# Performance work log

Hardware: AMD Instinct MI355X
Metric: run time of the kernel (lower is better)

## Reference

```python
import jax, jax.numpy as jnp
import numpy as np

WEIGHTS = {'seg': 1.0, 'grid': 0.5, 'baseline': 0.8, 'theta': 0.3, 'signal': 2.0}
IGNORE = 255


def _bce(p, t):
    # torch BCELoss: clamps log terms at -100
    lp = jnp.maximum(jnp.log(jnp.clip(p, 1e-12, 1.0)), -100.0)
    l1p = jnp.maximum(jnp.log(jnp.clip(1.0 - p, 1e-12, 1.0)), -100.0)
    return -(t * lp + (1.0 - t) * l1p).mean()


def _ce_ignore(logits, target):
    # logits (B,C,H,W), target (B,H,W) int; mean over target != 255
    logp = jax.nn.log_softmax(logits, axis=1)
    valid = target != IGNORE
    t_safe = jnp.where(valid, target, 0)
    nll = -jnp.take_along_axis(logp, t_safe[:, None].astype(jnp.int32), axis=1)[:, 0]
    return (nll * valid).sum() / jnp.maximum(valid.sum(), 1)


def _dice(logits, target, num_classes):
    p = jax.nn.softmax(logits, axis=1)                      # (B,C,H,W)
    oh = jax.nn.one_hot(target, num_classes, dtype=p.dtype) # (B,H,W,C)
    oh = jnp.transpose(oh, (0, 3, 1, 2))
    inter = (p * oh).sum(axis=(2, 3))
    union = p.sum(axis=(2, 3)) + oh.sum(axis=(2, 3))
    dice = (2.0 * inter + 1e-07) / (union + 1e-07)
    return 1.0 - dice.mean()


def _resize_bilinear_ac(x, out_h, out_w):
    # align_corners=True bilinear, x: (B,C,H,W)
    B, C, H, Wd = x.shape
    ys = jnp.linspace(0.0, H - 1.0, out_h)
    xs = jnp.linspace(0.0, Wd - 1.0, out_w)
    y0 = jnp.floor(ys).astype(jnp.int32); y1 = jnp.minimum(y0 + 1, H - 1); wy = (ys - y0).astype(x.dtype)
    x0 = jnp.floor(xs).astype(jnp.int32); x1 = jnp.minimum(x0 + 1, Wd - 1); wx = (xs - x0).astype(x.dtype)
    rows = x[:, :, y0, :] * (1 - wy)[None, None, :, None] + x[:, :, y1, :] * wy[None, None, :, None]
    out = rows[:, :, :, x0] * (1 - wx) + rows[:, :, :, x1] * wx
    return out


def _normalize_signal_masked(sig, mask):
    # sig, mask: (B,12,T); per-lead min/max normalize on valid region
    mf = mask.astype(sig.dtype)
    cnt = mf.sum(-1, keepdims=True)
    mn = jnp.min(jnp.where(mask, sig, jnp.inf), -1, keepdims=True)
    mx = jnp.max(jnp.where(mask, sig, -jnp.inf), -1, keepdims=True)
    rng = mx - mn
    ok = (cnt >= 2) & (rng >= 1e-06)
    mn_s = jnp.where(ok, mn, 0.0)
    rng_s = jnp.where(ok, rng, 1.0)
    norm = (2.0 * (sig - mn_s) / (rng_s + 1e-08) - 1.0) * mf
    return jnp.where(ok, norm, 0.0)


def _masked_mae(pred, target, mask):
    mf = mask.astype(pred.dtype)
    return (jnp.abs(pred - target) * mf).sum() / (mf.sum() + 1e-07)


def _masked_pearson(pred, target, mask):
    mf = mask.astype(pred.dtype)
    cnt = mf.sum(-1)                                   # (B,12)
    cs = jnp.maximum(cnt, 1.0)
    pm = (pred * mf).sum(-1) / cs
    tm = (target * mf).sum(-1) / cs
    pc = (pred - pm[..., None]) * mf
    tc = (target - tm[..., None]) * mf
    num = (pc * tc).sum(-1)
    ps = jnp.sqrt((pc ** 2).sum(-1) + 1e-06)
    ts = jnp.sqrt((tc ** 2).sum(-1) + 1e-06)
    corr = jnp.clip(num / (ps * ts + 1e-06), -1.0, 1.0)
    valid = (cnt >= 10).astype(pred.dtype)
    n_valid = valid.sum()
    avg = (corr * valid).sum() / jnp.maximum(n_valid, 1.0)
    return jnp.where(n_valid > 0, 1.0 - avg, 1.0)


def setup_inputs() -> dict:
    key = jax.random.key(0)
    ks = jax.random.split(key, 11)
    B, H, Wd, T = 8, 512, 512, 5000
    return {
        'wave_seg_pred': jax.random.normal(ks[0], (B, 13, H, Wd), jnp.float32),
        'wave_seg_target': jax.random.randint(ks[1], (B, H, Wd), 0, 13, jnp.int32),
        'grid_pred': jax.random.uniform(ks[2], (B, 1, H, Wd), jnp.float32),
        'grid_target': jax.random.uniform(ks[3], (B, 1, H, Wd), jnp.float32),
        'baseline_pred': jax.random.uniform(ks[4], (B, 12, H // 16, Wd // 16), jnp.float32),
        'baseline_target': jax.random.uniform(ks[5], (B, 12, H, Wd), jnp.float32),
        'theta_pred': jax.random.normal(ks[6], (B, 2, 3), jnp.float32),
        'theta_gt': jax.random.normal(ks[7], (B, 2, 3), jnp.float32),
        'signal_pred': jax.random.normal(ks[8], (B, 12, T), jnp.float32),
        'gt_signal': jax.random.normal(ks[9], (B, T, 12), jnp.float32),
        'signal_mask': jax.random.randint(ks[10], (B, T, 12), 0, 2, jnp.int32).astype(bool),
    }


def reference(wave_seg_pred, wave_seg_target, grid_pred, grid_target,
              baseline_pred, baseline_target, theta_pred, theta_gt,
              signal_pred, gt_signal, signal_mask):
    # seg
    seg = (_ce_ignore(wave_seg_pred, wave_seg_target)
           + _dice(wave_seg_pred, wave_seg_target, 13)) * WEIGHTS['seg']
    # grid
    inter = (grid_pred * grid_target).sum()
    union = grid_pred.sum() + grid_target.sum()
    grid = (_bce(grid_pred, grid_target)
            + (1.0 - (2.0 * inter + 1e-07) / (union + 1e-07))) * WEIGHTS['grid']
    # baseline
    Hp, Wp = baseline_pred.shape[2], baseline_pred.shape[3]
    bt = _resize_bilinear_ac(baseline_target, Hp, Wp)
    baseline = _bce(baseline_pred, bt) * WEIGHTS['baseline']
    # theta
    theta = jnp.abs(theta_pred - theta_gt).mean() * WEIGHTS['theta']
    # signal
    sig_t = jnp.swapaxes(gt_signal, 1, 2)     # (B,12,T)
    m = jnp.swapaxes(signal_mask, 1, 2)       # (B,12,T)
    pn = _normalize_signal_masked(signal_pred, m)
    tn = _normalize_signal_masked(sig_t, m)
    signal = (_masked_mae(pn, tn, m) + _masked_pearson(pn, tn, m)) * WEIGHTS['signal']
    total = seg + grid + baseline + theta + signal
    return jnp.stack([seg, grid, baseline, theta, signal, total])
```

## Files before the change

### kernel.cpp

```cpp
#include <hip/hip_runtime.h>
#include <math.h>

#define WS_SEG_NLL    0
#define WS_SEG_VALID  8
#define WS_INTER      16
#define WS_PSUM       120
#define WS_OHCNT      224
#define WS_GRID_BCE   328
#define WS_GRID_INTER 329
#define WS_GRID_PSUM  330
#define WS_GRID_TSUM  331
#define WS_BASE_BCE   332
#define WS_SIG_ABS    333
#define WS_SIG_CNT    334
#define WS_SIG_CORR   335
#define WS_SIG_NV     336
#define WS_MASK_FLAG  337
#define WS_DONE       338
#define WS_SIGSTATS   340
#define WS_FLOATS     820

#define SEG_NB   512
#define GRID_NB  256
#define BASE_NB  384
#define SIGA_NB  96
#define TOTAL_NB (SEG_NB + GRID_NB + BASE_NB + SIGA_NB)

#define AS_GLOBAL const __attribute__((address_space(1))) void*
#define AS_LDS    __attribute__((address_space(3))) void*

__device__ inline float wave_sum(float v) {
    #pragma unroll
    for (int o = 32; o > 0; o >>= 1) v += __shfl_down(v, o, 64);
    return v;
}

template <int OP>
__device__ inline float blk_red(float v, float* sb) {
    #pragma unroll
    for (int o = 32; o > 0; o >>= 1) {
        float u = __shfl_down(v, o, 64);
        v = (OP == 0) ? (v + u) : ((OP == 1) ? fminf(v, u) : fmaxf(v, u));
    }
    __syncthreads();
    if ((threadIdx.x & 63) == 0) sb[threadIdx.x >> 6] = v;
    __syncthreads();
    const int nw = blockDim.x >> 6;
    float r = sb[0];
    for (int w = 1; w < nw; w++) {
        float u = sb[w];
        r = (OP == 0) ? (r + u) : ((OP == 1) ? fminf(r, u) : fmaxf(r, u));
    }
    return r;
}

__device__ void seg_part(int sb_idx, const float* __restrict__ pred,
                         const int* __restrict__ tgt, float* __restrict__ ws) {
    const int b   = sb_idx >> 6;
    const int c64 = sb_idx & 63;
    const int HW  = 262144;
    const float* predf = pred + (size_t)b * 13 * HW;
    const int*   tgtb  = tgt + (size_t)b * HW;

    __shared__ alignas(16) float s_tile[28 * 256];
    int* s_tgt_i = (int*)&s_tile[26 * 256];
    __shared__ float s_inter[13];
    __shared__ float s_psum[13];
    __shared__ int   s_cnt[13];
    __shared__ float s_nll;
    __shared__ float s_nval;
    if (threadIdx.x < 13) { s_inter[threadIdx.x] = 0.f; s_psum[threadIdx.x] = 0.f; s_cnt[threadIdx.x] = 0; }
    if (threadIdx.x == 13) s_nll = 0.f;
    if (threadIdx.x == 14) s_nval = 0.f;

    const int lane = threadIdx.x & 63;
    const int wv   = threadIdx.x >> 6;

    float psum[13];
    #pragma unroll
    for (int c = 0; c < 13; c++) psum[c] = 0.f;
    float nll = 0.f, nval = 0.f;

    #pragma unroll 1
    for (int tile = 0; tile < 8; tile++) {
        const int px0 = c64 * 4096 + tile * 512;
        #pragma unroll
        for (int i = 0; i < 7; i++) {
            const int k = wv * 7 + i;
            const float* g;
            if (k < 26) g = predf + (size_t)(k >> 1) * HW + px0 + (k & 1) * 256;
            else        g = (const float*)(tgtb + px0 + (k - 26) * 256);
            g += lane * 4;
            __builtin_amdgcn_global_load_lds((AS_GLOBAL)g,
                                             (AS_LDS)&s_tile[k * 256], 16, 0, 0);
        }
        __syncthreads();

        #pragma unroll
        for (int kp = 0; kp < 2; kp++) {
            const int p = threadIdx.x + kp * 256;
            const int t = s_tgt_i[p];
            float x[13];
            #pragma unroll
            for (int c = 0; c < 13; c++) x[c] = s_tile[c * 512 + p];
            float m = x[0];
            #pragma unroll
            for (int c = 1; c < 13; c++) m = fmaxf(m, x[c]);
            float xt = x[0];
            #pragma unroll
            for (int c = 1; c < 13; c++) xt = (c == t) ? x[c] : xt;
            float se = 0.f;
            #pragma unroll
            for (int c = 0; c < 13; c++) { x[c] = __expf(x[c] - m); se += x[c]; }
            const float inv = __builtin_amdgcn_rcpf(se);
            #pragma unroll
            for (int c = 0; c < 13; c++) psum[c] += x[c] * inv;
            if ((unsigned)t < 13u) {
                atomicAdd(&s_inter[t], __expf(xt - m) * inv);
                atomicAdd(&s_cnt[t], 1);
                nll  += m + __logf(se) - xt;
                nval += 1.f;
            }
        }
        if (tile < 7) __syncthreads();
    }

    const bool lane0 = (lane == 0);
    #pragma unroll
    for (int c = 0; c < 13; c++) {
        float a = wave_sum(psum[c]);
        if (lane0) atomicAdd(&s_psum[c], a);
    }
    { float a = wave_sum(nll);  if (lane0) atomicAdd(&s_nll, a); }
    { float a = wave_sum(nval); if (lane0) atomicAdd(&s_nval, a); }
    __syncthreads();
    if (threadIdx.x < 13) {
        atomicAdd(&ws[WS_PSUM  + b * 13 + threadIdx.x], s_psum[threadIdx.x]);
        atomicAdd(&ws[WS_INTER + b * 13 + threadIdx.x], s_inter[threadIdx.x]);
        atomicAdd(&ws[WS_OHCNT + b * 13 + threadIdx.x], (float)s_cnt[threadIdx.x]);
    }
    if (threadIdx.x == 64) atomicAdd(&ws[WS_SEG_NLL + b],   s_nll);
    if (threadIdx.x == 65) atomicAdd(&ws[WS_SEG_VALID + b], s_nval);
}

__device__ void grid_part(int gb, const float4* __restrict__ gp,
                          const float4* __restrict__ gt, float* __restrict__ ws) {
    const int N4 = 2097152 / 4;
    float bce = 0.f, inter = 0.f, ps = 0.f, ts = 0.f;
    const int stride = GRID_NB * 256;
    for (int i = gb * 256 + threadIdx.x; i < N4; i += stride) {
        const float4 p4 = gp[i];
        const float4 t4 = gt[i];
        const float pa[4] = {p4.x, p4.y, p4.z, p4.w};
        const float ta[4] = {t4.x, t4.y, t4.z, t4.w};
        #pragma unroll
        for (int k = 0; k < 4; k++) {
            const float p = pa[k], t = ta[k];
            const float pc  = fminf(fmaxf(p, 1e-12f), 1.0f);
            const float qc  = fminf(fmaxf(1.f - p, 1e-12f), 1.0f);
            const float lp  = fmaxf(__logf(pc), -100.f);
            const float l1p = fmaxf(__logf(qc), -100.f);
            bce  -= t * lp + (1.f - t) * l1p;
            inter += p * t;
            ps += p;
            ts += t;
        }
    }
    __shared__ float s4[4];
    if (threadIdx.x < 4) s4[threadIdx.x] = 0.f;
    __syncthreads();
    const bool lane0 = (threadIdx.x & 63) == 0;
    { float a = wave_sum(bce);   if (lane0) atomicAdd(&s4[0], a); }
    { float a = wave_sum(inter); if (lane0) atomicAdd(&s4[1], a); }
    { float a = wave_sum(ps);    if (lane0) atomicAdd(&s4[2], a); }
    { float a = wave_sum(ts);    if (lane0) atomicAdd(&s4[3], a); }
    __syncthreads();
    if (threadIdx.x == 0) {
        atomicAdd(&ws[WS_GRID_BCE],   s4[0]);
        atomicAdd(&ws[WS_GRID_INTER], s4[1]);
        atomicAdd(&ws[WS_GRID_PSUM],  s4[2]);
        atomicAdd(&ws[WS_GRID_TSUM],  s4[3]);
    }
}

__device__ void base_part(int bb, const float* __restrict__ bp,
                          const float* __restrict__ bt, float* __restrict__ ws) {
    const int idx = bb * 256 + threadIdx.x;
    const int w  = idx & 31;
    const int h  = (idx >> 5) & 31;
    const int bc = idx >> 10;
    const float* img = bt + (size_t)bc * 262144;
    const float step = 511.0f / 31.0f;
    const float yy = h * step, xx = w * step;
    int y0 = (int)floorf(yy); int y1 = min(y0 + 1, 511); const float wy = yy - y0;
    int x0 = (int)floorf(xx); int x1 = min(x0 + 1, 511); const float wx = xx - x0;
    const float v00 = img[y0 * 512 + x0], v01 = img[y0 * 512 + x1];
    const float v10 = img[y1 * 512 + x0], v11 = img[y1 * 512 + x1];
    const float r0 = v00 * (1.f - wy) + v10 * wy;
    const float r1 = v01 * (1.f - wy) + v11 * wy;
    const float t  = r0 * (1.f - wx) + r1 * wx;
    const float p  = bp[idx];
    const float pc  = fminf(fmaxf(p, 1e-12f), 1.0f);
    const float qc  = fminf(fmaxf(1.f - p, 1e-12f), 1.0f);
    const float lp  = fmaxf(__logf(pc), -100.f);
    const float l1p = fmaxf(__logf(qc), -100.f);
    const float bce = -(t * lp + (1.f - t) * l1p);

    __shared__ float sb[4];
    const float s = blk_red<0>(bce, sb);
    if (threadIdx.x == 0) atomicAdd(&ws[WS_BASE_BCE], s);
}

__device__ void sigA_part(int sl, const float* __restrict__ sp,
                          const float* __restrict__ st, const void* __restrict__ mp,
                          float* __restrict__ ws) {
    const int T = 5000;
    const int b = sl / 12, l = sl % 12;
    const float* ps = sp + (size_t)(b * 12 + l) * T;
    const float* ts_base = st + (size_t)b * T * 12 + l;
    const int* mi = (const int*)mp;
    const unsigned char* mb = (const unsigned char*)mp;
    const size_t mbase = (size_t)b * T * 12 + l;

    __shared__ float sb[4];
    __shared__ int s_flag;
    if (threadIdx.x == 0) s_flag = 0;
    __syncthreads();
    int f = 0;
    for (int i = threadIdx.x; i < 3072; i += blockDim.x)
        if ((i & 3) && mb[i]) f = 1;
    if (__any(f) && (threadIdx.x & 63) == 0) atomicOr(&s_flag, 1);
    __syncthreads();
    const bool m32 = (s_flag == 0);

    float cnt = 0.f;
    float mnp = __builtin_inff(), mxp = -__builtin_inff();
    float mnt = __builtin_inff(), mxt = -__builtin_inff();
    for (int t = threadIdx.x; t < T; t += blockDim.x) {
        const bool m = m32 ? (mi[mbase + (size_t)t * 12] != 0)
                           : (mb[mbase + (size_t)t * 12] != 0);
        const float p  = ps[t];
        const float tv = ts_base[(size_t)t * 12];
        if (m) {
            cnt += 1.f;
            mnp = fminf(mnp, p);  mxp = fmaxf(mxp, p);
            mnt = fminf(mnt, tv); mxt = fmaxf(mxt, tv);
        }
    }
    cnt = blk_red<0>(cnt, sb);
    mnp = blk_red<1>(mnp, sb); mxp = blk_red<2>(mxp, sb);
    mnt = blk_red<1>(mnt, sb); mxt = blk_red<2>(mxt, sb);

    if (threadIdx.x == 0) {
        float* o = ws + WS_SIGSTATS + sl * 5;
        o[0] = cnt; o[1] = mnp; o[2] = mxp; o[3] = mnt; o[4] = mxt;
        if (sl == 0) ws[WS_MASK_FLAG] = m32 ? 1.0f : 0.0f;
    }
}

__global__ __launch_bounds__(256) void mega_kernel(
        const float* __restrict__ seg_pred, const int* __restrict__ seg_tgt,
        const float4* __restrict__ grid_pred, const float4* __restrict__ grid_tgt,
        const float* __restrict__ base_pred, const float* __restrict__ base_tgt,
        const float* __restrict__ sig_p, const float* __restrict__ sig_t,
        const void* __restrict__ maskp, float* __restrict__ ws) {
    const int bx = blockIdx.x;
    if (bx < SEG_NB) {
        seg_part(bx, seg_pred, seg_tgt, ws);
    } else if (bx < SEG_NB + GRID_NB) {
        grid_part(bx - SEG_NB, grid_pred, grid_tgt, ws);
    } else if (bx < SEG_NB + GRID_NB + BASE_NB) {
        base_part(bx - SEG_NB - GRID_NB, base_pred, base_tgt, ws);
    } else {
        sigA_part(bx - SEG_NB - GRID_NB - BASE_NB, sig_p, sig_t, maskp, ws);
    }
}

__global__ __launch_bounds__(256) void sigB_kernel(
        const float* __restrict__ sp, const float* __restrict__ st,
        const void* __restrict__ mp, const float* __restrict__ tp,
        const float* __restrict__ tg, float* __restrict__ ws,
        float* __restrict__ out) {
    const int T = 5000;
    const int sl = blockIdx.x;
    const int b = sl / 12, l = sl % 12;
    const float* ps = sp + (size_t)(b * 12 + l) * T;
    const float* ts_base = st + (size_t)b * T * 12 + l;
    const int* mi = (const int*)mp;
    const unsigned char* mb = (const unsigned char*)mp;
    const size_t mbase = (size_t)b * T * 12 + l;

    __shared__ float sb[4];
    const bool m32 = ws[WS_MASK_FLAG] > 0.5f;
    const float* stats = ws + WS_SIGSTATS + sl * 5;
    const float cnt = stats[0];
    const float mnp = stats[1], mxp = stats[2], mnt = stats[3], mxt = stats[4];

    const float rngp = mxp - mnp, rngt = mxt - mnt;
    const bool okp = (cnt >= 2.f) && (rngp >= 1e-6f);
    const bool okt = (cnt >= 2.f) && (rngt >= 1e-6f);
    const float mnp_s = okp ? mnp : 0.f, rp = okp ? rngp : 1.f;
    const float mnt_s = okt ? mnt : 0.f, rt = okt ? rngt : 1.f;
    const float invp = 2.f / (rp + 1e-8f), invt = 2.f / (rt + 1e-8f);

    float S_p = 0.f, S_t = 0.f, S_pt = 0.f, S_pp = 0.f, S_tt = 0.f, S_abs = 0.f;
    for (int t = threadIdx.x; t < T; t += blockDim.x) {
        const bool m = m32 ? (mi[mbase + (size_t)t * 12] != 0)
                           : (mb[mbase + (size_t)t * 12] != 0);
        const float p  = ps[t];
        const float tv = ts_base[(size_t)t * 12];
        const float pn = (m && okp) ? ((p  - mnp_s) * invp - 1.f) : 0.f;
        const float tn = (m && okt) ? ((tv - mnt_s) * invt - 1.f) : 0.f;
        S_p += pn; S_t += tn;
        S_pt += pn * tn; S_pp += pn * pn; S_tt += tn * tn;
        S_abs += m ? fabsf(pn - tn) : 0.f;
    }
    S_p  = blk_red<0>(S_p, sb);
    S_t  = blk_red<0>(S_t, sb);
    S_pt = blk_red<0>(S_pt, sb);
    S_pp = blk_red<0>(S_pp, sb);
    S_tt = blk_red<0>(S_tt, sb);
    S_abs = blk_red<0>(S_abs, sb);

    __shared__ int s_last;
    if (threadIdx.x == 0) {
        const float cs = fmaxf(cnt, 1.f);
        const float pm = S_p / cs, tm = S_t / cs;
        const float num = S_pt - pm * S_t - tm * S_p + pm * tm * cnt;
        const float psd = sqrtf(fmaxf(S_pp - 2.f * pm * S_p + pm * pm * cnt, 0.f) + 1e-6f);
        const float tsd = sqrtf(fmaxf(S_tt - 2.f * tm * S_t + tm * tm * cnt, 0.f) + 1e-6f);
        float corr = num / (psd * tsd + 1e-6f);
        corr = fminf(fmaxf(corr, -1.f), 1.f);
        const float valid = (cnt >= 10.f) ? 1.f : 0.f;
        atomicAdd(&ws[WS_SIG_ABS],  S_abs);
        atomicAdd(&ws[WS_SIG_CNT],  cnt);
        atomicAdd(&ws[WS_SIG_CORR], corr * valid);
        atomicAdd(&ws[WS_SIG_NV],   valid);
        __threadfence();
        const int old = atomicAdd((int*)(ws + WS_DONE), 1);
        s_last = (old == 95) ? 1 : 0;
    }
    __syncthreads();
    if (!s_last) return;

    __shared__ float s_d, s_nll, s_nv, s_th;
    if (threadIdx.x == 0) { s_d = 0.f; s_nll = 0.f; s_nv = 0.f; s_th = 0.f; }
    __syncthreads();
    const int t = threadIdx.x;
    float d = 0.f, nll = 0.f, nv = 0.f, th = 0.f;
    if (t < 104) {
        const float it = ws[WS_INTER + t], p = ws[WS_PSUM + t], oh = ws[WS_OHCNT + t];
        d = (2.f * it + 1e-7f) / (p + oh + 1e-7f);
    }
    if (t < 8) { nll = ws[WS_SEG_NLL + t]; nv = ws[WS_SEG_VALID + t]; }
    if (t < 48) th = fabsf(tp[t] - tg[t]);
    d = wave_sum(d); nll = wave_sum(nll); nv = wave_sum(nv); th = wave_sum(th);
    if ((t & 63) == 0) {
        atomicAdd(&s_d, d); atomicAdd(&s_nll, nll);
        atomicAdd(&s_nv, nv); atomicAdd(&s_th, th);
    }
    __syncthreads();
    if (t == 0) {
        const float ce = s_nll / fmaxf(s_nv, 1.f);
        const float seg = (ce + (1.f - s_d / 104.f)) * 1.0f;
        const float bce_g = ws[WS_GRID_BCE] / 2097152.f;
        const float gd = 1.f - (2.f * ws[WS_GRID_INTER] + 1e-7f) /
                               (ws[WS_GRID_PSUM] + ws[WS_GRID_TSUM] + 1e-7f);
        const float grid = (bce_g + gd) * 0.5f;
        const float base = (ws[WS_BASE_BCE] / 98304.f) * 0.8f;
        const float theta = (s_th / 48.f) * 0.3f;
        const float sabs = atomicAdd(&ws[WS_SIG_ABS],  0.f);
        const float scnt = atomicAdd(&ws[WS_SIG_CNT],  0.f);
        const float scor = atomicAdd(&ws[WS_SIG_CORR], 0.f);
        const float snv  = atomicAdd(&ws[WS_SIG_NV],   0.f);
        const float mae = sabs / (scnt + 1e-7f);
        const float pear = (snv > 0.f) ? (1.f - scor / fmaxf(snv, 1.f)) : 1.f;
        const float sig = (mae + pear) * 2.0f;
        const float total = seg + grid + base + theta + sig;
        out[0] = seg; out[1] = grid; out[2] = base; out[3] = theta; out[4] = sig;
        out[5] = total;
    }
}

extern "C" void kernel_launch(void* const* d_in, const int* in_sizes, int n_in,
                              void* d_out, int out_size, void* d_ws, size_t ws_size,
                              hipStream_t stream) {
    const float* seg_pred  = (const float*)d_in[0];
    const int*   seg_tgt   = (const int*)d_in[1];
    const float* grid_pred = (const float*)d_in[2];
    const float* grid_tgt  = (const float*)d_in[3];
    const float* base_pred = (const float*)d_in[4];
    const float* base_tgt  = (const float*)d_in[5];
    const float* theta_p   = (const float*)d_in[6];
    const float* theta_g   = (const float*)d_in[7];
    const float* sig_p     = (const float*)d_in[8];
    const float* sig_t     = (const float*)d_in[9];
    const void*  maskp     = d_in[10];
    float* ws  = (float*)d_ws;
    float* out = (float*)d_out;

    hipMemsetAsync(d_ws, 0, WS_FLOATS * sizeof(float), stream);
    mega_kernel<<<TOTAL_NB, 256, 0, stream>>>(
        seg_pred, seg_tgt,
        (const float4*)grid_pred, (const float4*)grid_tgt,
        base_pred, base_tgt, sig_p, sig_t, maskp, ws);
    sigB_kernel<<<96, 256, 0, stream>>>(sig_p, sig_t, maskp, theta_p, theta_g, ws, out);
}
```

Baseline: 288.3 us.

## Split seg work into one 512-pixel tile per block with plain vector loads

The segmentation part now launches eight times as many blocks, each handling a single 512-pixel tile instead of looping over eight tiles. The async global-to-LDS loads are replaced with ordinary float4 loads that are stored to shared memory. The target-class probability is also taken from the already computed softmax rather than from a second exp. This aims to expose more parallelism and latency hiding across blocks, at the cost of more per-block setup and more global atomics for the final reduction.

```diff
diff --git a/kernel.cpp b/kernel.cpp
--- a/kernel.cpp
+++ b/kernel.cpp
@@ -20,14 +20,11 @@
 #define WS_SIGSTATS   340
 #define WS_FLOATS     820
 
-#define SEG_NB   512
+#define SEG_NB   4096
 #define GRID_NB  256
 #define BASE_NB  384
 #define SIGA_NB  96
 #define TOTAL_NB (SEG_NB + GRID_NB + BASE_NB + SIGA_NB)
-
-#define AS_GLOBAL const __attribute__((address_space(1))) void*
-#define AS_LDS    __attribute__((address_space(3))) void*
 
 __device__ inline float wave_sum(float v) {
     #pragma unroll
@@ -56,14 +53,16 @@
 
 __device__ void seg_part(int sb_idx, const float* __restrict__ pred,
                          const int* __restrict__ tgt, float* __restrict__ ws) {
-    const int b   = sb_idx >> 6;
-    const int c64 = sb_idx & 63;
-    const int HW  = 262144;
+    const int b  = sb_idx >> 9;
+    const int xb = sb_idx & 511;
+    const int px0 = xb * 512;
+    const int HW = 262144;
     const float* predf = pred + (size_t)b * 13 * HW;
     const int*   tgtb  = tgt + (size_t)b * HW;
 
-    __shared__ alignas(16) float s_tile[28 * 256];
-    int* s_tgt_i = (int*)&s_tile[26 * 256];
+    __shared__ alignas(16) float4 s_flat[1792];
+    float* s_tile = (float*)s_flat;
+    const int* s_tgt_i = (const int*)(s_flat + 1664);
     __shared__ float s_inter[13];
     __shared__ float s_psum[13];
     __shared__ int   s_cnt[13];
@@ -73,58 +72,60 @@
     if (threadIdx.x == 13) s_nll = 0.f;
     if (threadIdx.x == 14) s_nval = 0.f;
 
-    const int lane = threadIdx.x & 63;
-    const int wv   = threadIdx.x >> 6;
+    #pragma unroll
+    for (int i = 0; i < 7; i++) {
+        const int q = threadIdx.x + i * 256;
+        const int f = q * 4;
+        float4 v;
+        if (q < 1664) {
+            const int c = f >> 9;
+            const int p = f & 511;
+            v = *(const float4*)(predf + (size_t)c * HW + px0 + p);
+        } else {
+            v = *(const float4*)(tgtb + px0 + (f - 6656));
+        }
+        s_flat[q] = v;
+    }
+    __syncthreads();
 
     float psum[13];
     #pragma unroll
     for (int c = 0; c < 13; c++) psum[c] = 0.f;
     float nll = 0.f, nval = 0.f;
 
-    #pragma unroll 1
-    for (int tile = 0; tile < 8; tile++) {
-        const int px0 = c64 * 4096 + tile * 512;
-        #pragma unroll
-        for (int i = 0; i < 7; i++) {
-            const int k = wv * 7 + i;
-            const float* g;
-            if (k < 26) g = predf + (size_t)(k >> 1) * HW + px0 + (k & 1) * 256;
-            else        g = (const float*)(tgtb + px0 + (k - 26) * 256);
-            g += lane * 4;
-            __builtin_amdgcn_global_load_lds((AS_GLOBAL)g,
-                                             (AS_LDS)&s_tile[k * 256], 16, 0, 0);
+    #pragma unroll
+    for (int kp = 0; kp < 2; kp++) {
+        const int p = threadIdx.x + kp * 256;
+        const int t = s_tgt_i[p];
+        float x[13];
+        #pragma unroll
+        for (int c = 0; c < 13; c++) x[c] = s_tile[c * 512 + p];
+        float m = x[0];
+        #pragma unroll
+        for (int c = 1; c < 13; c++) m = fmaxf(m, x[c]);
+        float xt = x[0];
+        #pragma unroll
+        for (int c = 1; c < 13; c++) xt = (c == t) ? x[c] : xt;
+        float se = 0.f;
+        #pragma unroll
+        for (int c = 0; c < 13; c++) { x[c] = __expf(x[c] - m); se += x[c]; }
+        const float inv = __builtin_amdgcn_rcpf(se);
+        float pt = 0.f;
+        #pragma unroll
+        for (int c = 0; c < 13; c++) {
+            const float pr = x[c] * inv;
+            psum[c] += pr;
+            pt = (c == t) ? pr : pt;
         }
-        __syncthreads();
-
-        #pragma unroll
-        for (int kp = 0; kp < 2; kp++) {
-            const int p = threadIdx.x + kp * 256;
-            const int t = s_tgt_i[p];
-            float x[13];
-            #pragma unroll
-            for (int c = 0; c < 13; c++) x[c] = s_tile[c * 512 + p];
-            float m = x[0];
-            #pragma unroll
-            for (int c = 1; c < 13; c++) m = fmaxf(m, x[c]);
-            float xt = x[0];
-            #pragma unroll
-            for (int c = 1; c < 13; c++) xt = (c == t) ? x[c] : xt;
-            float se = 0.f;
-            #pragma unroll
-            for (int c = 0; c < 13; c++) { x[c] = __expf(x[c] - m); se += x[c]; }
-            const float inv = __builtin_amdgcn_rcpf(se);
-            #pragma unroll
-            for (int c = 0; c < 13; c++) psum[c] += x[c] * inv;
-            if ((unsigned)t < 13u) {
-                atomicAdd(&s_inter[t], __expf(xt - m) * inv);
-                atomicAdd(&s_cnt[t], 1);
-                nll  += m + __logf(se) - xt;
-                nval += 1.f;
-            }
+        if ((unsigned)t < 13u) {
+            atomicAdd(&s_inter[t], pt);
+            atomicAdd(&s_cnt[t], 1);
+            nll  += m + __logf(se) - xt;
+            nval += 1.f;
         }
-        if (tile < 7) __syncthreads();
-    }
-
+    }
+
+    const int lane = threadIdx.x & 63;
     const bool lane0 = (lane == 0);
     #pragma unroll
     for (int c = 0; c < 13; c++) {
```

Result: slower. 324.7 us (+12.6%).
